# Optimization experiments

Measured on AMD Instinct MI355X. Metric: run time of the kernel, lower is better.

The kernel has to match this reference:

```python
import jax, jax.numpy as jnp
import numpy as np

B, S, D, H = 2, 2048, 1024, 16
FF = 4 * D
DH = D // H
WINDOW, NGLOBAL = 128, 16
EPS = 1e-5
NEG = -1e9


def build_mask():
    # additive mask [S, S]: 0 where attention allowed, NEG otherwise
    i = jnp.arange(S)[:, None]
    j = jnp.arange(S)[None, :]
    allowed = (jnp.abs(i - j) <= WINDOW) | (j < NGLOBAL) | (i < NGLOBAL)
    allowed = allowed & (j <= i)  # causal
    return jnp.where(allowed, 0.0, NEG).astype(jnp.float32)


def layer_norm(x, g, b):
    mu = jnp.mean(x, axis=-1, keepdims=True)
    var = jnp.mean((x - mu) ** 2, axis=-1, keepdims=True)
    return (x - mu) * jax.lax.rsqrt(var + EPS) * g + b


def setup_inputs() -> dict:
    key = jax.random.key(0)
    ks = jax.random.split(key, 10)
    s = 0.02
    return {
        "x": jax.random.normal(ks[0], (B, S, D), jnp.float32),
        "attention_mask": jnp.ones((B, S), jnp.int32),
        "w_in": jax.random.normal(ks[1], (3 * D, D), jnp.float32) * s,
        "b_in": jnp.zeros((3 * D,), jnp.float32),
        "w_out": jax.random.normal(ks[2], (D, D), jnp.float32) * s,
        "b_out": jnp.zeros((D,), jnp.float32),
        "g_ln1": jnp.ones((D,), jnp.float32),
        "b_ln1": jnp.zeros((D,), jnp.float32),
        "g_ln2": jnp.ones((D,), jnp.float32),
        "b_ln2": jnp.zeros((D,), jnp.float32),
        "w1": jax.random.normal(ks[3], (FF, D), jnp.float32) * s,
        "b1": jnp.zeros((FF,), jnp.float32),
        "w2": jax.random.normal(ks[4], (D, FF), jnp.float32) * s,
        "b2": jnp.zeros((D,), jnp.float32),
    }


def reference(x, attention_mask, w_in, b_in, w_out, b_out,
              g_ln1, b_ln1, g_ln2, b_ln2, w1, b1, w2, b2):
    # --- attention sub-block (pre-LN) ---
    h = layer_norm(x, g_ln1, b_ln1)
    qkv = h @ w_in.T + b_in                       # [B,S,3D]
    q, k, v = jnp.split(qkv, 3, axis=-1)
    q = q.reshape(B, S, H, DH)
    k = k.reshape(B, S, H, DH)
    v = v.reshape(B, S, H, DH)
    scores = jnp.einsum('bihd,bjhd->bhij', q, k) / np.sqrt(DH)
    mask = build_mask()[None, None]               # [1,1,S,S]
    kp = jnp.where(attention_mask == 0, NEG, 0.0)[:, None, None, :]
    attn = jax.nn.softmax(scores + mask + kp, axis=-1)
    o = jnp.einsum('bhij,bjhd->bihd', attn, v).reshape(B, S, D)
    x = x + (o @ w_out.T + b_out)
    # --- MLP sub-block (pre-LN) ---
    h = layer_norm(x, g_ln2, b_ln2)
    h = jax.nn.gelu(h @ w1.T + b1, approximate=False) @ w2.T + b2
    return x + h
```

## Files before the change

### kernel.cpp

```cpp
#include <hip/hip_runtime.h>
#include <cstdint>
#include <cstddef>


using bf16x8 = __attribute__((ext_vector_type(8))) short;
using f32x4  = __attribute__((ext_vector_type(4))) float;

#define B_  2
#define S_  2048
#define D_  1024
#define H_  16
#define DH_ 64
#define FF_ 4096

static __device__ __forceinline__ unsigned short f2bf(float f) {
    union { float f; unsigned u; } v; v.f = f;
    unsigned r = (v.u + 0x7FFFu + ((v.u >> 16) & 1u)) >> 16;
    return (unsigned short)r;
}

__global__ __launch_bounds__(256) void cvt4_kernel(const float* __restrict__ a, const float* __restrict__ b,
                                                   const float* __restrict__ c, const float* __restrict__ d,
                                                   unsigned short* __restrict__ oa, unsigned short* __restrict__ ob,
                                                   unsigned short* __restrict__ oc, unsigned short* __restrict__ od) {
    const int i = blockIdx.x * blockDim.x + threadIdx.x;
    const float* src; unsigned short* dst; int off;
    if (i < 786432)       { src = a; dst = oa; off = i; }
    else if (i < 1048576) { src = b; dst = ob; off = i - 786432; }
    else if (i < 2097152) { src = c; dst = oc; off = i - 1048576; }
    else                  { src = d; dst = od; off = i - 2097152; }
    const float4 v = *(const float4*)&src[(size_t)off * 4];
    ushort4 o = make_ushort4(f2bf(v.x), f2bf(v.y), f2bf(v.z), f2bf(v.w));
    *(ushort4*)&dst[(size_t)off * 4] = o;
}

__global__ __launch_bounds__(256) void ln_kernel(const float* __restrict__ x,
                                                 const float* __restrict__ g,
                                                 const float* __restrict__ bb,
                                                 unsigned short* __restrict__ out) {
    const int row = blockIdx.x;
    const int t = threadIdx.x;
    const float4 v = *(const float4*)&x[(size_t)row * D_ + t * 4];
    float s  = v.x + v.y + v.z + v.w;
    float s2 = v.x * v.x + v.y * v.y + v.z * v.z + v.w * v.w;
#pragma unroll
    for (int off = 32; off > 0; off >>= 1) {
        s  += __shfl_down(s,  off);
        s2 += __shfl_down(s2, off);
    }
    __shared__ float red[8];
    const int w = t >> 6;
    if ((t & 63) == 0) { red[w] = s; red[4 + w] = s2; }
    __syncthreads();
    s  = red[0] + red[1] + red[2] + red[3];
    s2 = red[4] + red[5] + red[6] + red[7];
    const float mu  = s * (1.f / D_);
    const float var = s2 * (1.f / D_) - mu * mu;
    const float rs  = rsqrtf(var + 1e-5f);
    const int c = t * 4;
    ushort4 o = make_ushort4(f2bf((v.x - mu) * rs * g[c + 0] + bb[c + 0]),
                             f2bf((v.y - mu) * rs * g[c + 1] + bb[c + 1]),
                             f2bf((v.z - mu) * rs * g[c + 2] + bb[c + 2]),
                             f2bf((v.w - mu) * rs * g[c + 3] + bb[c + 3]));
    *(ushort4*)&out[(size_t)row * D_ + c] = o;
}

template <int BN, int NSUB, int HAS_RES, int GELU, int OUT_BF16>
__global__ __launch_bounds__(256) void gemm_bt(const unsigned short* __restrict__ A,
                                               const unsigned short* __restrict__ W,
                                               const float* __restrict__ bias,
                                               const float* __restrict__ res,
                                               void* __restrict__ outp,
                                               int M, int N, int K) {
    constexpr int NF = BN / 32;
    __shared__ unsigned short As[NSUB][128 * 32];
    __shared__ unsigned short Bs[NSUB][BN * 32];
    const int t = threadIdx.x;
    const int lane = t & 63, w = t >> 6;
    const int m0 = blockIdx.x * 128, n0 = blockIdx.y * BN;
    const int wr = w >> 1, wc = w & 1;
    const int r16 = lane & 15, g4 = lane >> 4;
    const int kq = g4 * 8;

    f32x4 acc[4][NF];
    const f32x4 zero = {0.f, 0.f, 0.f, 0.f};
#pragma unroll
    for (int i = 0; i < 4; ++i)
#pragma unroll
        for (int j = 0; j < NF; ++j) acc[i][j] = zero;

    const int lrow  = lane >> 2;
    const int lkoff = (lane & 3) * 8;

    const unsigned short* a0 = A + (size_t)(m0 + w * 32 + lrow) * K + lkoff;
    const unsigned short* a1 = a0 + (size_t)16 * K;
    const unsigned short* b0;
    const unsigned short* b1 = nullptr;
    if (BN == 128) {
        b0 = W + (size_t)(n0 + w * 32 + lrow) * K + lkoff;
        b1 = b0 + (size_t)16 * K;
    } else {
        b0 = W + (size_t)(n0 + w * 16 + lrow) * K + lkoff;
    }

    for (int kt = 0; kt < K; kt += NSUB * 32) {
#pragma unroll
        for (int s = 0; s < NSUB; ++s) {
            const int ko = kt + s * 32;
            __builtin_amdgcn_global_load_lds((const unsigned int*)(a0 + ko),
                                             (unsigned int*)&As[s][(w * 32) * 32], 16, 0, 0);
            __builtin_amdgcn_global_load_lds((const unsigned int*)(a1 + ko),
                                             (unsigned int*)&As[s][(w * 32 + 16) * 32], 16, 0, 0);
            if (BN == 128) {
                __builtin_amdgcn_global_load_lds((const unsigned int*)(b0 + ko),
                                                 (unsigned int*)&Bs[s][(w * 32) * 32], 16, 0, 0);
                __builtin_amdgcn_global_load_lds((const unsigned int*)(b1 + ko),
                                                 (unsigned int*)&Bs[s][(w * 32 + 16) * 32], 16, 0, 0);
            } else {
                __builtin_amdgcn_global_load_lds((const unsigned int*)(b0 + ko),
                                                 (unsigned int*)&Bs[s][(w * 16) * 32], 16, 0, 0);
            }
        }
        __syncthreads();
#pragma unroll
        for (int s = 0; s < NSUB; ++s) {
            bf16x8 af[4], bfr[NF];
#pragma unroll
            for (int i = 0; i < 4; ++i) af[i]  = *(const bf16x8*)&As[s][(wr * 64 + i * 16 + r16) * 32 + kq];
#pragma unroll
            for (int j = 0; j < NF; ++j) bfr[j] = *(const bf16x8*)&Bs[s][(wc * (BN / 2) + j * 16 + r16) * 32 + kq];
#pragma unroll
            for (int i = 0; i < 4; ++i)
#pragma unroll
                for (int j = 0; j < NF; ++j)
                    acc[i][j] = __builtin_amdgcn_mfma_f32_16x16x32_bf16(af[i], bfr[j], acc[i][j], 0, 0, 0);
        }
        __syncthreads();
    }

#pragma unroll
    for (int i = 0; i < 4; ++i) {
        const int row = m0 + wr * 64 + i * 16 + g4 * 4;
#pragma unroll
        for (int j = 0; j < NF; ++j) {
            const int col = n0 + wc * (BN / 2) + j * 16 + r16;
            const float bi = bias[col];
#pragma unroll
            for (int r = 0; r < 4; ++r) {
                float v = acc[i][j][r] + bi;
                if (GELU) v = 0.5f * v * (1.f + erff(v * 0.70710678118f));
                if (HAS_RES) v += res[(size_t)(row + r) * N + col];
                if (OUT_BF16) ((unsigned short*)outp)[(size_t)(row + r) * N + col] = f2bf(v);
                else          ((float*)outp)[(size_t)(row + r) * N + col] = v;
            }
        }
    }
}

__global__ __launch_bounds__(256) void attn_kernel(const unsigned short* __restrict__ qkv,
                                                   unsigned short* __restrict__ o) {
    __shared__ unsigned short Kl[64 * 64];
    __shared__ unsigned short Vt[64 * 64];
    __shared__ unsigned short Pl[4][16 * 64];
    const int t = threadIdx.x, lane = t & 63, w = t >> 6;
    const int qb = blockIdx.x & 31;
    const int bh = blockIdx.x >> 5;
    const int b = bh >> 4, h = bh & 15;
    const int i0 = qb * 64;
    const int r16 = lane & 15, g4 = lane >> 4;

    const int qrow = i0 + w * 16 + r16;
    const size_t qoff = ((size_t)(b * S_ + qrow)) * (3 * D_) + h * DH_;
    const bf16x8 qa0 = *(const bf16x8*)&qkv[qoff + g4 * 8];
    const bf16x8 qa1 = *(const bf16x8*)&qkv[qoff + 32 + g4 * 8];

    float m_r[4], l_r[4];
    f32x4 oacc[4];
    const f32x4 zero = {0.f, 0.f, 0.f, 0.f};
#pragma unroll
    for (int r = 0; r < 4; ++r) { m_r[r] = -INFINITY; l_r[r] = 0.f; }
#pragma unroll
    for (int d = 0; d < 4; ++d) oacc[d] = zero;

    const int ks = (i0 >= 192) ? (i0 - 128) : 0;
    const int nw = (i0 + 64 - ks) >> 6;
    const int ntiles = nw + (ks > 0 ? 1 : 0);

    const int srow = t >> 2;
    const int scol = (t & 3) * 16;

    for (int idx = 0; idx < ntiles; ++idx) {
        const int kt = (ks == 0) ? (idx << 6) : (idx == 0 ? 0 : ks + ((idx - 1) << 6));
        {
            const size_t base = ((size_t)(b * S_ + kt + srow)) * (3 * D_) + D_ + h * DH_ + scol;
            const float4 k0 = *(const float4*)&qkv[base];
            const float4 k1 = *(const float4*)&qkv[base + 8];
            *(float4*)&Kl[srow * 64 + scol]     = k0;
            *(float4*)&Kl[srow * 64 + scol + 8] = k1;
            const float4 v0 = *(const float4*)&qkv[base + D_];
            const float4 v1 = *(const float4*)&qkv[base + D_ + 8];
            const unsigned short* pv0 = (const unsigned short*)&v0;
            const unsigned short* pv1 = (const unsigned short*)&v1;
#pragma unroll
            for (int e = 0; e < 8; ++e) {
                Vt[(scol + e) * 64 + srow]     = pv0[e];
                Vt[(scol + 8 + e) * 64 + srow] = pv1[e];
            }
        }
        __syncthreads();

        f32x4 sc[4];
#pragma unroll
        for (int ct = 0; ct < 4; ++ct) {
            sc[ct] = zero;
            bf16x8 kb = *(const bf16x8*)&Kl[(ct * 16 + r16) * 64 + g4 * 8];
            sc[ct] = __builtin_amdgcn_mfma_f32_16x16x32_bf16(qa0, kb, sc[ct], 0, 0, 0);
            kb = *(const bf16x8*)&Kl[(ct * 16 + r16) * 64 + 32 + g4 * 8];
            sc[ct] = __builtin_amdgcn_mfma_f32_16x16x32_bf16(qa1, kb, sc[ct], 0, 0, 0);
        }

        const int ib = i0 + w * 16 + g4 * 4;
        float pr[4][4];
#pragma unroll
        for (int r = 0; r < 4; ++r) {
            const int i = ib + r;
#pragma unroll
            for (int ct = 0; ct < 4; ++ct) {
                const int j = kt + ct * 16 + r16;
                const float s = sc[ct][r] * 0.125f;
                pr[ct][r] = ((j <= i) && ((i - j) <= 128 || j < 16)) ? s : -1e30f;
            }
        }
#pragma unroll
        for (int r = 0; r < 4; ++r) {
            float tm = fmaxf(fmaxf(pr[0][r], pr[1][r]), fmaxf(pr[2][r], pr[3][r]));
            tm = fmaxf(tm, __shfl_xor(tm, 1, 16));
            tm = fmaxf(tm, __shfl_xor(tm, 2, 16));
            tm = fmaxf(tm, __shfl_xor(tm, 4, 16));
            tm = fmaxf(tm, __shfl_xor(tm, 8, 16));
            const float mn = fmaxf(m_r[r], tm);
            const float f = expf(m_r[r] - mn);
            m_r[r] = mn;
            const float p0 = expf(pr[0][r] - mn);
            const float p1 = expf(pr[1][r] - mn);
            const float p2 = expf(pr[2][r] - mn);
            const float p3 = expf(pr[3][r] - mn);
            float rsum = (p0 + p1) + (p2 + p3);
            rsum += __shfl_xor(rsum, 1, 16);
            rsum += __shfl_xor(rsum, 2, 16);
            rsum += __shfl_xor(rsum, 4, 16);
            rsum += __shfl_xor(rsum, 8, 16);
            l_r[r] = l_r[r] * f + rsum;
#pragma unroll
            for (int d = 0; d < 4; ++d) oacc[d][r] *= f;
            const int prow = (g4 * 4 + r) * 64;
            Pl[w][prow + r16]      = f2bf(p0);
            Pl[w][prow + 16 + r16] = f2bf(p1);
            Pl[w][prow + 32 + r16] = f2bf(p2);
            Pl[w][prow + 48 + r16] = f2bf(p3);
        }
        const bf16x8 pa0 = *(const bf16x8*)&Pl[w][r16 * 64 + g4 * 8];
        const bf16x8 pa1 = *(const bf16x8*)&Pl[w][r16 * 64 + 32 + g4 * 8];
#pragma unroll
        for (int d = 0; d < 4; ++d) {
            bf16x8 vb = *(const bf16x8*)&Vt[(d * 16 + r16) * 64 + g4 * 8];
            oacc[d] = __builtin_amdgcn_mfma_f32_16x16x32_bf16(pa0, vb, oacc[d], 0, 0, 0);
            vb = *(const bf16x8*)&Vt[(d * 16 + r16) * 64 + 32 + g4 * 8];
            oacc[d] = __builtin_amdgcn_mfma_f32_16x16x32_bf16(pa1, vb, oacc[d], 0, 0, 0);
        }
        __syncthreads();
    }

#pragma unroll
    for (int d = 0; d < 4; ++d)
#pragma unroll
        for (int r = 0; r < 4; ++r) {
            const int row = i0 + w * 16 + g4 * 4 + r;
            o[((size_t)(b * S_ + row)) * D_ + h * DH_ + d * 16 + r16] = f2bf(oacc[d][r] / l_r[r]);
        }
}

extern "C" void kernel_launch(void* const* d_in, const int* in_sizes, int n_in,
                              void* d_out, int out_size, void* d_ws, size_t ws_size,
                              hipStream_t stream) {
    const float* x     = (const float*)d_in[0];
    const float* w_in  = (const float*)d_in[2];
    const float* b_in  = (const float*)d_in[3];
    const float* w_out = (const float*)d_in[4];
    const float* b_out = (const float*)d_in[5];
    const float* g_ln1 = (const float*)d_in[6];
    const float* b_ln1 = (const float*)d_in[7];
    const float* g_ln2 = (const float*)d_in[8];
    const float* b_ln2 = (const float*)d_in[9];
    const float* w1    = (const float*)d_in[10];
    const float* b1    = (const float*)d_in[11];
    const float* w2    = (const float*)d_in[12];
    const float* b2    = (const float*)d_in[13];
    float* out = (float*)d_out;

    const int M = B_ * S_;
    char* ws = (char*)d_ws;
    unsigned short* w_in_b  = (unsigned short*)ws;
    unsigned short* w_out_b = w_in_b  + (size_t)3 * D_ * D_;
    unsigned short* w1_b    = w_out_b + (size_t)D_ * D_;
    unsigned short* w2_b    = w1_b    + (size_t)FF_ * D_;
    unsigned short* h1      = w2_b    + (size_t)D_ * FF_;
    unsigned short* qkvb    = h1      + (size_t)M * D_;
    unsigned short* m1      = h1;
    unsigned short* ob      = qkvb    + (size_t)M * 3 * D_;
    unsigned short* h2      = ob      + (size_t)M * D_;
    float*          x2      = out;

    cvt4_kernel<<<12288, 256, 0, stream>>>(w_in, w_out, w1, w2, w_in_b, w_out_b, w1_b, w2_b);

    ln_kernel<<<M, 256, 0, stream>>>(x, g_ln1, b_ln1, h1);
    gemm_bt<128, 2, 0, 0, 1><<<dim3(M / 128, (3 * D_) / 128), 256, 0, stream>>>(h1, w_in_b, b_in, nullptr, qkvb, M, 3 * D_, D_);
    attn_kernel<<<B_ * H_ * (S_ / 64), 256, 0, stream>>>(qkvb, ob);
    gemm_bt<64, 4, 1, 0, 0><<<dim3(M / 128, D_ / 64), 256, 0, stream>>>(ob, w_out_b, b_out, x, x2, M, D_, D_);
    ln_kernel<<<M, 256, 0, stream>>>(x2, g_ln2, b_ln2, h2);
    gemm_bt<128, 2, 0, 1, 1><<<dim3(M / 128, FF_ / 128), 256, 0, stream>>>(h2, w1_b, b1, nullptr, m1, M, FF_, D_);
    gemm_bt<64, 4, 1, 0, 0><<<dim3(M / 128, D_ / 64), 256, 0, stream>>>(m1, w2_b, b2, x2, out, M, D_, FF_);

    (void)in_sizes; (void)n_in; (void)out_size; (void)ws_size;
}
```

Measured before the change: 338.8 us.

## Merge weight conversion with first LayerNorm and add 256x128 tile GEMM

```diff
diff --git a/kernel.cpp b/kernel.cpp
--- a/kernel.cpp
+++ b/kernel.cpp
@@ -19,19 +19,49 @@
     return (unsigned short)r;
 }
 
-__global__ __launch_bounds__(256) void cvt4_kernel(const float* __restrict__ a, const float* __restrict__ b,
-                                                   const float* __restrict__ c, const float* __restrict__ d,
+__global__ __launch_bounds__(256) void prep_kernel(const float* __restrict__ wa, const float* __restrict__ wb,
+                                                   const float* __restrict__ wc, const float* __restrict__ wd,
                                                    unsigned short* __restrict__ oa, unsigned short* __restrict__ ob,
-                                                   unsigned short* __restrict__ oc, unsigned short* __restrict__ od) {
-    const int i = blockIdx.x * blockDim.x + threadIdx.x;
-    const float* src; unsigned short* dst; int off;
-    if (i < 786432)       { src = a; dst = oa; off = i; }
-    else if (i < 1048576) { src = b; dst = ob; off = i - 786432; }
-    else if (i < 2097152) { src = c; dst = oc; off = i - 1048576; }
-    else                  { src = d; dst = od; off = i - 2097152; }
-    const float4 v = *(const float4*)&src[(size_t)off * 4];
-    ushort4 o = make_ushort4(f2bf(v.x), f2bf(v.y), f2bf(v.z), f2bf(v.w));
-    *(ushort4*)&dst[(size_t)off * 4] = o;
+                                                   unsigned short* __restrict__ oc, unsigned short* __restrict__ od,
+                                                   const float* __restrict__ x, const float* __restrict__ g,
+                                                   const float* __restrict__ bb, unsigned short* __restrict__ h1) {
+    if (blockIdx.x < 12288) {
+        const int i = blockIdx.x * blockDim.x + threadIdx.x;
+        const float* src; unsigned short* dst; int off;
+        if (i < 786432)       { src = wa; dst = oa; off = i; }
+        else if (i < 1048576) { src = wb; dst = ob; off = i - 786432; }
+        else if (i < 2097152) { src = wc; dst = oc; off = i - 1048576; }
+        else                  { src = wd; dst = od; off = i - 2097152; }
+        const float4 v = *(const float4*)&src[(size_t)off * 4];
+        ushort4 o = make_ushort4(f2bf(v.x), f2bf(v.y), f2bf(v.z), f2bf(v.w));
+        *(ushort4*)&dst[(size_t)off * 4] = o;
+        return;
+    }
+    const int row = blockIdx.x - 12288;
+    const int t = threadIdx.x;
+    const float4 v = *(const float4*)&x[(size_t)row * D_ + t * 4];
+    float s  = v.x + v.y + v.z + v.w;
+    float s2 = v.x * v.x + v.y * v.y + v.z * v.z + v.w * v.w;
+#pragma unroll
+    for (int off = 32; off > 0; off >>= 1) {
+        s  += __shfl_down(s,  off);
+        s2 += __shfl_down(s2, off);
+    }
+    __shared__ float red[8];
+    const int w = t >> 6;
+    if ((t & 63) == 0) { red[w] = s; red[4 + w] = s2; }
+    __syncthreads();
+    s  = red[0] + red[1] + red[2] + red[3];
+    s2 = red[4] + red[5] + red[6] + red[7];
+    const float mu  = s * (1.f / D_);
+    const float var = s2 * (1.f / D_) - mu * mu;
+    const float rs  = rsqrtf(var + 1e-5f);
+    const int c = t * 4;
+    ushort4 o = make_ushort4(f2bf((v.x - mu) * rs * g[c + 0] + bb[c + 0]),
+                             f2bf((v.y - mu) * rs * g[c + 1] + bb[c + 1]),
+                             f2bf((v.z - mu) * rs * g[c + 2] + bb[c + 2]),
+                             f2bf((v.w - mu) * rs * g[c + 3] + bb[c + 3]));
+    *(ushort4*)&h1[(size_t)row * D_ + c] = o;
 }
 
 __global__ __launch_bounds__(256) void ln_kernel(const float* __restrict__ x,
@@ -63,6 +93,80 @@
                              f2bf((v.z - mu) * rs * g[c + 2] + bb[c + 2]),
                              f2bf((v.w - mu) * rs * g[c + 3] + bb[c + 3]));
     *(ushort4*)&out[(size_t)row * D_ + c] = o;
+}
+
+template <int GELU>
+__global__ __launch_bounds__(512) void gemm_bt2(const unsigned short* __restrict__ A,
+                                                const unsigned short* __restrict__ W,
+                                                const float* __restrict__ bias,
+                                                unsigned short* __restrict__ outp,
+                                                int M, int N, int K) {
+    __shared__ unsigned short As[2][256 * 32];
+    __shared__ unsigned short Bs[2][128 * 32];
+    const int t = threadIdx.x;
+    const int lane = t & 63, w = t >> 6;
+    const int m0 = blockIdx.x * 256, n0 = blockIdx.y * 128;
+    const int wrow = w >> 1, wcol = w & 1;
+    const int r16 = lane & 15, g4 = lane >> 4;
+    const int kq = g4 * 8;
+
+    f32x4 acc[4][4];
+    const f32x4 zero = {0.f, 0.f, 0.f, 0.f};
+#pragma unroll
+    for (int i = 0; i < 4; ++i)
+#pragma unroll
+        for (int j = 0; j < 4; ++j) acc[i][j] = zero;
+
+    const int lrow  = lane >> 2;
+    const int lkoff = (lane & 3) * 8;
+
+    const unsigned short* a0 = A + (size_t)(m0 + w * 32 + lrow) * K + lkoff;
+    const unsigned short* a1 = a0 + (size_t)16 * K;
+    const unsigned short* b0 = W + (size_t)(n0 + w * 16 + lrow) * K + lkoff;
+
+    for (int kt = 0; kt < K; kt += 64) {
+#pragma unroll
+        for (int s = 0; s < 2; ++s) {
+            const int ko = kt + s * 32;
+            __builtin_amdgcn_global_load_lds((const unsigned int*)(a0 + ko),
+                                             (unsigned int*)&As[s][(w * 32) * 32], 16, 0, 0);
+            __builtin_amdgcn_global_load_lds((const unsigned int*)(a1 + ko),
+                                             (unsigned int*)&As[s][(w * 32 + 16) * 32], 16, 0, 0);
+            __builtin_amdgcn_global_load_lds((const unsigned int*)(b0 + ko),
+                                             (unsigned int*)&Bs[s][(w * 16) * 32], 16, 0, 0);
+        }
+        __syncthreads();
+#pragma unroll
+        for (int s = 0; s < 2; ++s) {
+            bf16x8 af[4], bfr[4];
+#pragma unroll
+            for (int i = 0; i < 4; ++i) af[i]  = *(const bf16x8*)&As[s][(wrow * 64 + i * 16 + r16) * 32 + kq];
+#pragma unroll
+            for (int j = 0; j < 4; ++j) bfr[j] = *(const bf16x8*)&Bs[s][(wcol * 64 + j * 16 + r16) * 32 + kq];
+#pragma unroll
+            for (int i = 0; i < 4; ++i)
+#pragma unroll
+                for (int j = 0; j < 4; ++j)
+                    acc[i][j] = __builtin_amdgcn_mfma_f32_16x16x32_bf16(af[i], bfr[j], acc[i][j], 0, 0, 0);
+        }
+        __syncthreads();
+    }
+
+#pragma unroll
+    for (int i = 0; i < 4; ++i) {
+        const int row = m0 + wrow * 64 + i * 16 + g4 * 4;
+#pragma unroll
+        for (int j = 0; j < 4; ++j) {
+            const int col = n0 + wcol * 64 + j * 16 + r16;
+            const float bi = bias[col];
+#pragma unroll
+            for (int r = 0; r < 4; ++r) {
+                float v = acc[i][j][r] + bi;
+                if (GELU) v = 0.5f * v * (1.f + erff(v * 0.70710678118f));
+                outp[(size_t)(row + r) * N + col] = f2bf(v);
+            }
+        }
+    }
 }
 
 template <int BN, int NSUB, int HAS_RES, int GELU, int OUT_BF16>
@@ -311,14 +415,13 @@
     unsigned short* h2      = ob      + (size_t)M * D_;
     float*          x2      = out;
 
-    cvt4_kernel<<<12288, 256, 0, stream>>>(w_in, w_out, w1, w2, w_in_b, w_out_b, w1_b, w2_b);
-
-    ln_kernel<<<M, 256, 0, stream>>>(x, g_ln1, b_ln1, h1);
-    gemm_bt<128, 2, 0, 0, 1><<<dim3(M / 128, (3 * D_) / 128), 256, 0, stream>>>(h1, w_in_b, b_in, nullptr, qkvb, M, 3 * D_, D_);
+    prep_kernel<<<12288 + M, 256, 0, stream>>>(w_in, w_out, w1, w2, w_in_b, w_out_b, w1_b, w2_b,
+                                               x, g_ln1, b_ln1, h1);
+    gemm_bt2<0><<<dim3(M / 256, (3 * D_) / 128), 512, 0, stream>>>(h1, w_in_b, b_in, qkvb, M, 3 * D_, D_);
     attn_kernel<<<B_ * H_ * (S_ / 64), 256, 0, stream>>>(qkvb, ob);
     gemm_bt<64, 4, 1, 0, 0><<<dim3(M / 128, D_ / 64), 256, 0, stream>>>(ob, w_out_b, b_out, x, x2, M, D_, D_);
     ln_kernel<<<M, 256, 0, stream>>>(x2, g_ln2, b_ln2, h2);
-    gemm_bt<128, 2, 0, 1, 1><<<dim3(M / 128, FF_ / 128), 256, 0, stream>>>(h2, w1_b, b1, nullptr, m1, M, FF_, D_);
+    gemm_bt2<1><<<dim3(M / 256, FF_ / 128), 512, 0, stream>>>(h2, w1_b, b1, m1, M, FF_, D_);
     gemm_bt<64, 4, 1, 0, 0><<<dim3(M / 128, D_ / 64), 256, 0, stream>>>(m1, w2_b, b2, x2, out, M, D_, FF_);
 
     (void)in_sizes; (void)n_in; (void)out_size; (void)ws_size;
```

New measurement: 311.9 us. 7.9% less time.
